# Kernel tuning notes

Hardware: AMD Instinct MI355X
Metric: run time of the kernel (lower is better)

The kernel has to match this reference:

```python
import jax, jax.numpy as jnp
import numpy as np
from jax import lax

H = 256        # hidden_size
T = 576        # history length (PERIOD*24)
F_T = 24       # future steps
M = 32         # m_features
B = 256        # batch
PERIOD = T // 24
E = 2 * H      # encoder output dim (bidirectional)
EPS = 1e-6     # torch PairwiseDistance eps


def setup_inputs() -> dict:
    key = jax.random.key(0)
    ks = jax.random.split(key, 16)
    rn = lambda k, sh, s=1.0: jax.random.normal(k, sh, jnp.float32) * s
    return {
        "input_encoded": rn(ks[0], (B, T, E)),
        "feature_history1": rn(ks[1], (B, T, M)),
        "y_history": rn(ks[2], (B, T, 1)),               # unused by forward (matches torch)
        "feature_future1": rn(ks[3], (B, F_T, M)),
        "hidden": rn(ks[4], (2, B, H), 0.1),
        "cell": rn(ks[5], (2, B, H), 0.1),
        # attn_layer: Linear(2H+M -> T), Tanh, Linear(T -> T)
        "attn_W1": rn(ks[6], (T, E + M), 0.05), "attn_b1": jnp.zeros((T,), jnp.float32),
        "attn_W2": rn(ks[7], (T, T), 0.05),     "attn_b2": jnp.zeros((T,), jnp.float32),
        # bidirectional 1-layer LSTM, stacked over direction d in {fwd, bwd}
        "W_ih": rn(ks[8], (2, 4 * H, E + M), 0.05),
        "W_hh": rn(ks[9], (2, 4 * H, H), 0.05),
        "b_ih": jnp.zeros((2, 4 * H), jnp.float32),
        "b_hh": jnp.zeros((2, 4 * H), jnp.float32),
        # fc_final: Linear(2H -> H), ReLU, Linear(H -> 1)
        "fcf_W1": rn(ks[10], (H, E), 0.05), "fcf_b1": jnp.zeros((H,), jnp.float32),
        "fcf_W2": rn(ks[11], (1, H), 0.05), "fcf_b2": jnp.zeros((1,), jnp.float32),
    }


def reference(input_encoded, feature_history1, y_history, feature_future1,
              hidden, cell, attn_W1, attn_b1, attn_W2, attn_b2,
              W_ih, W_hh, b_ih, b_hh, fcf_W1, fcf_b1, fcf_W2, fcf_b2):
    b = input_encoded.shape[0]
    # --- period-similarity weights alpha (computed once) ---
    fh = feature_history1.reshape(b, PERIOD, 24, M)                 # [B,period,24,M]
    # pairwise L2 distance between future [B,24,1,M] and history hours [B,24,period,M]
    diff = feature_future1[:, :, None, :] - fh.transpose(0, 2, 1, 3)  # [B,24,period,M]
    dist = jnp.sqrt(jnp.sum((diff + EPS) ** 2, axis=-1))            # [B,24,period]
    dp = 1.0 / jnp.sum(dist, axis=2)                                # rsqrt(.)**2 == 1/x; [B,24]
    alpha = jax.nn.softmax(dp, axis=1)                              # [B,24] (period==24)
    enc = input_encoded.reshape(b, PERIOD, 24, E)                   # [B,period,24,E]
    bias = (b_ih + b_hh)[:, None, :]                                # [2,1,4H]

    def step(carry, ff_t):                                          # ff_t: [B,M]
        h, c = carry                                                # each [2,B,H]
        x = jnp.concatenate([h[0], h[1], ff_t], axis=1)             # [B,2H+M]
        a = jnp.tanh(x @ attn_W1.T + attn_b1) @ attn_W2.T + attn_b2
        a = jax.nn.softmax(a, axis=1)                               # [B,T]
        w = a.reshape(b, PERIOD, 24)                                # [B,period,24]
        # context: sum attention-weighted encodings over each day, then alpha over periods
        ctx = jnp.einsum('bpk,bpke,bp->be', w, enc, alpha)          # [B,E]
        inp = jnp.concatenate([ctx, ff_t], axis=1)                  # [B,2H+M]
        gates = (jnp.einsum('bi,dgi->dbg', inp, W_ih)
                 + jnp.einsum('dbh,dgh->dbg', h, W_hh) + bias)      # [2,B,4H]
        i_g, f_g, g_g, o_g = jnp.split(gates, 4, axis=-1)           # torch gate order i,f,g,o
        c_new = jax.nn.sigmoid(f_g) * c + jax.nn.sigmoid(i_g) * jnp.tanh(g_g)
        h_new = jax.nn.sigmoid(o_g) * jnp.tanh(c_new)               # [2,B,H]
        hh = jnp.concatenate([h_new[0], h_new[1]], axis=1)          # [B,2H]
        y = jax.nn.relu(hh @ fcf_W1.T + fcf_b1) @ fcf_W2.T + fcf_b2  # [B,1]
        return (h_new, c_new), y

    _, ys = lax.scan(step, (hidden, cell), jnp.transpose(feature_future1, (1, 0, 2)))
    return jnp.transpose(ys, (1, 0, 2))                             # [B,f_T,1]
```

## Files before the change

### kernel.cpp

```cpp
#include <hip/hip_runtime.h>
#include <math.h>

#define B_ 256
#define T_ 576
#define FT_ 24
#define M_ 32
#define H_ 256
#define E_ 512
#define KX_ 544
#define G_ 1024
#define ND_ 2048
#define EPS_ 1e-6f

typedef __attribute__((ext_vector_type(8))) short bf8;
typedef __attribute__((ext_vector_type(4))) float f4;

__device__ __forceinline__ float bf2f(unsigned short s) {
    union { unsigned u; float f; } c; c.u = ((unsigned)s) << 16; return c.f;
}
__device__ __forceinline__ short f2bf(float f) {
    union { float f; unsigned u; } c; c.f = f;
    unsigned r = c.u + 0x7fffu + ((c.u >> 16) & 1u);
    return (short)(r >> 16);
}
__device__ __forceinline__ float sigm(float x) { return 1.f / (1.f + expf(-x)); }

__global__ __launch_bounds__(64) void k_alpha(const float* __restrict__ ff,
                                              const float* __restrict__ fhist,
                                              float* __restrict__ alpha) {
    int b = blockIdx.x;
    int t = threadIdx.x;
    float dp = 0.f;
    if (t < 24) {
        float fv[M_];
        const float* fp = ff + (b * FT_ + t) * M_;
        #pragma unroll
        for (int m = 0; m < M_; m++) fv[m] = fp[m];
        float dist = 0.f;
        for (int p = 0; p < 24; p++) {
            const float* hp = fhist + (b * T_ + p * 24 + t) * M_;
            float s = 0.f;
            #pragma unroll
            for (int m = 0; m < M_; m++) { float d = fv[m] - hp[m] + EPS_; s += d * d; }
            dist += sqrtf(s);
        }
        dp = 1.f / dist;
    }
    float v = (t < 24) ? dp : -INFINITY;
    float mx = v;
    for (int off = 32; off; off >>= 1) mx = fmaxf(mx, __shfl_xor(mx, off));
    float e = (t < 24) ? expf(dp - mx) : 0.f;
    float sm = e;
    for (int off = 32; off; off >>= 1) sm += __shfl_xor(sm, off);
    if (t < 24) alpha[b * 24 + t] = e / sm;
}

__global__ __launch_bounds__(256) void k_cast4(const float* __restrict__ src,
                                               short* __restrict__ dst, int n4) {
    int i = blockIdx.x * 256 + threadIdx.x;
    if (i < n4) {
        float4 v = ((const float4*)src)[i];
        short4 o;
        o.x = f2bf(v.x); o.y = f2bf(v.y); o.z = f2bf(v.z); o.w = f2bf(v.w);
        ((short4*)dst)[i] = o;
    }
}

__global__ __launch_bounds__(256) void k_init(const float* __restrict__ hidden,
                                              const float* __restrict__ cell,
                                              const float* __restrict__ ff,
                                              short* __restrict__ x, short* __restrict__ hb,
                                              float* __restrict__ c) {
    int i = blockIdx.x * 256 + threadIdx.x;
    int d = i >> 16, b = (i >> 8) & 255, j = i & 255;
    float h = hidden[i];
    short hv = f2bf(h);
    hb[i] = hv;
    x[b * KX_ + d * H_ + j] = hv;
    c[i] = cell[i];
    if (d == 0 && j < M_) x[b * KX_ + E_ + j] = f2bf(ff[(b * FT_ + 0) * M_ + j]);
}

template <int EPI>
__global__ __launch_bounds__(256) void k_gemm(const short* __restrict__ A, int lda, int K,
                                              const short* __restrict__ W,
                                              const float* __restrict__ bias,
                                              void* __restrict__ out, int ldc) {
    __shared__ short As[64][40];
    __shared__ short Bs[64][40];
    int n0 = blockIdx.x * 64, m0 = blockIdx.y * 64;
    int tid = threadIdx.x, lane = tid & 63, w = tid >> 6;
    int wm = (w & 1) * 32, wn = (w >> 1) * 32;
    int r = tid >> 2, cg = (tid & 3) * 8;
    f4 acc[2][2] = {};
    int nch = K / 32;
    int4 pa = *(const int4*)(A + (m0 + r) * lda + cg);
    int4 pb = *(const int4*)(W + (n0 + r) * K + cg);
    for (int kc = 0; kc < nch; kc++) {
        *(int4*)&As[r][cg] = pa;
        *(int4*)&Bs[r][cg] = pb;
        __syncthreads();
        if (kc + 1 < nch) {
            int ko = (kc + 1) * 32 + cg;
            pa = *(const int4*)(A + (m0 + r) * lda + ko);
            pb = *(const int4*)(W + (n0 + r) * K + ko);
        }
        int fr = lane & 15, fk = (lane >> 4) * 8;
        bf8 a0 = *(const bf8*)&As[wm + fr][fk];
        bf8 a1 = *(const bf8*)&As[wm + 16 + fr][fk];
        bf8 b0 = *(const bf8*)&Bs[wn + fr][fk];
        bf8 b1 = *(const bf8*)&Bs[wn + 16 + fr][fk];
        acc[0][0] = __builtin_amdgcn_mfma_f32_16x16x32_bf16(a0, b0, acc[0][0], 0, 0, 0);
        acc[0][1] = __builtin_amdgcn_mfma_f32_16x16x32_bf16(a0, b1, acc[0][1], 0, 0, 0);
        acc[1][0] = __builtin_amdgcn_mfma_f32_16x16x32_bf16(a1, b0, acc[1][0], 0, 0, 0);
        acc[1][1] = __builtin_amdgcn_mfma_f32_16x16x32_bf16(a1, b1, acc[1][1], 0, 0, 0);
        __syncthreads();
    }
    int colb = n0 + wn + (lane & 15);
    int rowb = m0 + wm + (lane >> 4) * 4;
    #pragma unroll
    for (int im = 0; im < 2; im++)
        #pragma unroll
        for (int in = 0; in < 2; in++) {
            int col = colb + in * 16;
            float bv = bias[col];
            #pragma unroll
            for (int q = 0; q < 4; q++) {
                int row = rowb + im * 16 + q;
                float v = acc[im][in][q] + bv;
                if (EPI == 0)      ((short*)out)[row * ldc + col] = f2bf(tanhf(v));
                else if (EPI == 1) ((float*)out)[row * ldc + col] = v;
                else               ((float*)out)[row * ldc + col] = fmaxf(v, 0.f);
            }
        }
}

template <int BF16E>
__global__ __launch_bounds__(256) void k_ctx(const float* __restrict__ logits,
                                             const float* __restrict__ alpha,
                                             const short* __restrict__ encb,
                                             const float* __restrict__ encf,
                                             float* __restrict__ ctxp) {
    int b = blockIdx.x >> 2, s = blockIdx.x & 3;
    int tid = threadIdx.x;
    __shared__ float wt[T_];
    __shared__ float red[4];
    const float* lg = logits + b * T_;
    float l0 = lg[tid], l1 = lg[tid + 256];
    float l2 = (tid < 64) ? lg[tid + 512] : -INFINITY;
    float mx = fmaxf(fmaxf(l0, l1), l2);
    for (int off = 32; off; off >>= 1) mx = fmaxf(mx, __shfl_xor(mx, off));
    if ((tid & 63) == 0) red[tid >> 6] = mx;
    __syncthreads();
    mx = fmaxf(fmaxf(red[0], red[1]), fmaxf(red[2], red[3]));
    float e0 = expf(l0 - mx), e1 = expf(l1 - mx);
    float e2 = (tid < 64) ? expf(l2 - mx) : 0.f;
    float sm = e0 + e1 + e2;
    for (int off = 32; off; off >>= 1) sm += __shfl_xor(sm, off);
    __syncthreads();
    if ((tid & 63) == 0) red[tid >> 6] = sm;
    __syncthreads();
    float inv = 1.f / (red[0] + red[1] + red[2] + red[3]);
    const float* al = alpha + b * 24;
    wt[tid]       = e0 * inv * al[tid / 24];
    wt[tid + 256] = e1 * inv * al[(tid + 256) / 24];
    if (tid < 64) wt[tid + 512] = e2 * inv * al[(tid + 512) / 24];
    __syncthreads();
    float a0 = 0.f, a1 = 0.f;
    int t0 = s * (T_ / 4);
    if (BF16E) {
        const unsigned* ep = (const unsigned*)(encb + (b * T_ + t0) * E_) + tid;
        for (int t = 0; t < T_ / 4; t++) {
            float wv = wt[t0 + t];
            unsigned u = ep[t * (E_ / 2)];
            a0 += wv * bf2f((unsigned short)(u & 0xffffu));
            a1 += wv * bf2f((unsigned short)(u >> 16));
        }
    } else {
        const float2* ep = (const float2*)(encf + ((size_t)b * T_ + t0) * E_) + tid;
        for (int t = 0; t < T_ / 4; t++) {
            float wv = wt[t0 + t];
            float2 u = ep[t * (E_ / 2)];
            a0 += wv * u.x;
            a1 += wv * u.y;
        }
    }
    float* cp = ctxp + (s * B_ + b) * E_;
    cp[2 * tid] = a0;
    cp[2 * tid + 1] = a1;
}

__global__ __launch_bounds__(256) void k_gates(const float* __restrict__ ctxp,
                                               const float* __restrict__ ff, int step,
                                               const short* __restrict__ hb,
                                               const short* __restrict__ Wih,
                                               const short* __restrict__ Whh,
                                               float* __restrict__ gates) {
    __shared__ short As[64][40];
    __shared__ short Bs[64][40];
    int n0 = blockIdx.x * 64, m0 = blockIdx.y * 64;
    int tid = threadIdx.x, lane = tid & 63, w = tid >> 6;
    int wm = (w & 1) * 32, wn = (w >> 1) * 32;
    int r = tid >> 2, cg = (tid & 3) * 8;
    int b = m0 + r;
    f4 acc[2][2] = {};
    int fr = lane & 15, fk = (lane >> 4) * 8;
    for (int kc = 0; kc < KX_ / 32; kc++) {
        int k = kc * 32 + cg;
        short av[8];
        if (k < E_) {
            const float* c0 = ctxp + b * E_ + k;
            #pragma unroll
            for (int j = 0; j < 8; j++) {
                float v = c0[j] + c0[B_ * E_ + j] + c0[2 * B_ * E_ + j] + c0[3 * B_ * E_ + j];
                av[j] = f2bf(v);
            }
        } else {
            const float* fp = ff + (b * FT_ + step) * M_ + (k - E_);
            #pragma unroll
            for (int j = 0; j < 8; j++) av[j] = f2bf(fp[j]);
        }
        *(int4*)&As[r][cg] = *(int4*)av;
        *(int4*)&Bs[r][cg] = *(const int4*)(Wih + (n0 + r) * KX_ + k);
        __syncthreads();
        bf8 a0 = *(const bf8*)&As[wm + fr][fk];
        bf8 a1 = *(const bf8*)&As[wm + 16 + fr][fk];
        bf8 b0 = *(const bf8*)&Bs[wn + fr][fk];
        bf8 b1 = *(const bf8*)&Bs[wn + 16 + fr][fk];
        acc[0][0] = __builtin_amdgcn_mfma_f32_16x16x32_bf16(a0, b0, acc[0][0], 0, 0, 0);
        acc[0][1] = __builtin_amdgcn_mfma_f32_16x16x32_bf16(a0, b1, acc[0][1], 0, 0, 0);
        acc[1][0] = __builtin_amdgcn_mfma_f32_16x16x32_bf16(a1, b0, acc[1][0], 0, 0, 0);
        acc[1][1] = __builtin_amdgcn_mfma_f32_16x16x32_bf16(a1, b1, acc[1][1], 0, 0, 0);
        __syncthreads();
    }
    int d = n0 >> 10;
    const short* A2 = hb + d * B_ * H_;
    for (int kc = 0; kc < H_ / 32; kc++) {
        int k = kc * 32 + cg;
        *(int4*)&As[r][cg] = *(const int4*)(A2 + b * H_ + k);
        *(int4*)&Bs[r][cg] = *(const int4*)(Whh + (n0 + r) * H_ + k);
        __syncthreads();
        bf8 a0 = *(const bf8*)&As[wm + fr][fk];
        bf8 a1 = *(const bf8*)&As[wm + 16 + fr][fk];
        bf8 b0 = *(const bf8*)&Bs[wn + fr][fk];
        bf8 b1 = *(const bf8*)&Bs[wn + 16 + fr][fk];
        acc[0][0] = __builtin_amdgcn_mfma_f32_16x16x32_bf16(a0, b0, acc[0][0], 0, 0, 0);
        acc[0][1] = __builtin_amdgcn_mfma_f32_16x16x32_bf16(a0, b1, acc[0][1], 0, 0, 0);
        acc[1][0] = __builtin_amdgcn_mfma_f32_16x16x32_bf16(a1, b0, acc[1][0], 0, 0, 0);
        acc[1][1] = __builtin_amdgcn_mfma_f32_16x16x32_bf16(a1, b1, acc[1][1], 0, 0, 0);
        __syncthreads();
    }
    int colb = n0 + wn + (lane & 15);
    int rowb = m0 + wm + (lane >> 4) * 4;
    #pragma unroll
    for (int im = 0; im < 2; im++)
        #pragma unroll
        for (int in = 0; in < 2; in++)
            #pragma unroll
            for (int q = 0; q < 4; q++)
                gates[(rowb + im * 16 + q) * ND_ + colb + in * 16] = acc[im][in][q];
}

__global__ __launch_bounds__(256) void k_lstm(const float* __restrict__ gates,
                                              const float* __restrict__ bih,
                                              const float* __restrict__ bhh,
                                              const float* __restrict__ ff, int step,
                                              float* __restrict__ c, short* __restrict__ hb,
                                              short* __restrict__ x) {
    int i = blockIdx.x * 256 + threadIdx.x;
    int d = i >> 16, b = (i >> 8) & 255, j = i & 255;
    int gb = b * ND_ + d * G_;
    int bb = d * G_;
    float ig = gates[gb + j]       + bih[bb + j]       + bhh[bb + j];
    float fg = gates[gb + 256 + j] + bih[bb + 256 + j] + bhh[bb + 256 + j];
    float gg = gates[gb + 512 + j] + bih[bb + 512 + j] + bhh[bb + 512 + j];
    float og = gates[gb + 768 + j] + bih[bb + 768 + j] + bhh[bb + 768 + j];
    float cv = c[i];
    float cn = sigm(fg) * cv + sigm(ig) * tanhf(gg);
    float hn = sigm(og) * tanhf(cn);
    c[i] = cn;
    short hv = f2bf(hn);
    hb[i] = hv;
    x[b * KX_ + d * H_ + j] = hv;
    if (d == 0 && j < M_ && step + 1 < FT_)
        x[b * KX_ + E_ + j] = f2bf(ff[(b * FT_ + step + 1) * M_ + j]);
}

__global__ __launch_bounds__(256) void k_fc2(const float* __restrict__ z,
                                             const float* __restrict__ w2,
                                             const float* __restrict__ b2,
                                             float* __restrict__ out, int step) {
    int b = blockIdx.x * 4 + (threadIdx.x >> 6);
    int lane = threadIdx.x & 63;
    const float* zr = z + b * H_;
    float s = zr[lane] * w2[lane] + zr[lane + 64] * w2[lane + 64] +
              zr[lane + 128] * w2[lane + 128] + zr[lane + 192] * w2[lane + 192];
    for (int off = 32; off; off >>= 1) s += __shfl_xor(s, off);
    if (lane == 0) out[b * FT_ + step] = s + b2[0];
}

extern "C" void kernel_launch(void* const* d_in, const int* in_sizes, int n_in,
                              void* d_out, int out_size, void* d_ws, size_t ws_size,
                              hipStream_t stream) {
    (void)in_sizes; (void)n_in; (void)out_size;
    const float* enc_f  = (const float*)d_in[0];
    const float* fhist  = (const float*)d_in[1];
    const float* ff     = (const float*)d_in[3];
    const float* hidden = (const float*)d_in[4];
    const float* cell   = (const float*)d_in[5];
    const float* aW1    = (const float*)d_in[6];
    const float* ab1    = (const float*)d_in[7];
    const float* aW2    = (const float*)d_in[8];
    const float* ab2    = (const float*)d_in[9];
    const float* Wih    = (const float*)d_in[10];
    const float* Whh    = (const float*)d_in[11];
    const float* bih    = (const float*)d_in[12];
    const float* bhh    = (const float*)d_in[13];
    const float* fW1    = (const float*)d_in[14];
    const float* fb1    = (const float*)d_in[15];
    const float* fW2    = (const float*)d_in[16];
    const float* fb2    = (const float*)d_in[17];
    float* out = (float*)d_out;

    char* p = (char*)d_ws;
    auto take = [&](size_t n) { char* r = p; p += (n + 255) & ~(size_t)255; return r; };
    float* alpha = (float*)take(B_ * 24 * 4);
    short* xb    = (short*)take(B_ * KX_ * 2);
    short* hb    = (short*)take(2 * B_ * H_ * 2);
    float* cbuf  = (float*)take(2 * B_ * H_ * 4);
    short* s1    = (short*)take(B_ * T_ * 2);
    float* logit = (float*)take(B_ * T_ * 4);
    float* ctxp  = (float*)take(4 * B_ * E_ * 4);
    float* gates = (float*)take(B_ * ND_ * 4);
    float* z     = (float*)take(B_ * H_ * 4);
    short* W1b   = (short*)take(T_ * KX_ * 2);
    short* W2b   = (short*)take(T_ * T_ * 2);
    short* Wihb  = (short*)take(ND_ * KX_ * 2);
    short* Whhb  = (short*)take(ND_ * H_ * 2);
    short* fW1b  = (short*)take(H_ * E_ * 2);
    short* encb  = (short*)take((size_t)B_ * T_ * E_ * 2);
    size_t full_need = (size_t)(p - (char*)d_ws);
    bool use_encb = ws_size >= full_need;

    k_alpha<<<B_, 64, 0, stream>>>(ff, fhist, alpha);
    k_cast4<<<(T_ * KX_ / 4 + 255) / 256, 256, 0, stream>>>(aW1, W1b, T_ * KX_ / 4);
    k_cast4<<<(T_ * T_ / 4 + 255) / 256, 256, 0, stream>>>(aW2, W2b, T_ * T_ / 4);
    k_cast4<<<(ND_ * KX_ / 4 + 255) / 256, 256, 0, stream>>>(Wih, Wihb, ND_ * KX_ / 4);
    k_cast4<<<(ND_ * H_ / 4 + 255) / 256, 256, 0, stream>>>(Whh, Whhb, ND_ * H_ / 4);
    k_cast4<<<(H_ * E_ / 4 + 255) / 256, 256, 0, stream>>>(fW1, fW1b, H_ * E_ / 4);
    if (use_encb)
        k_cast4<<<(B_ * T_ * E_ / 4 + 255) / 256, 256, 0, stream>>>(enc_f, encb, B_ * T_ * E_ / 4);
    k_init<<<(2 * B_ * H_) / 256, 256, 0, stream>>>(hidden, cell, ff, xb, hb, cbuf);

    for (int step = 0; step < FT_; step++) {
        k_gemm<0><<<dim3(T_ / 64, B_ / 64), 256, 0, stream>>>(xb, KX_, KX_, W1b, ab1, s1, T_);
        k_gemm<1><<<dim3(T_ / 64, B_ / 64), 256, 0, stream>>>(s1, T_, T_, W2b, ab2, logit, T_);
        if (use_encb)
            k_ctx<1><<<B_ * 4, 256, 0, stream>>>(logit, alpha, encb, enc_f, ctxp);
        else
            k_ctx<0><<<B_ * 4, 256, 0, stream>>>(logit, alpha, encb, enc_f, ctxp);
        k_gates<<<dim3(ND_ / 64, B_ / 64), 256, 0, stream>>>(ctxp, ff, step, hb, Wihb, Whhb, gates);
        k_lstm<<<(2 * B_ * H_) / 256, 256, 0, stream>>>(gates, bih, bhh, ff, step, cbuf, hb, xb);
        k_gemm<3><<<dim3(H_ / 64, B_ / 64), 256, 0, stream>>>(xb, KX_, E_, fW1b, fb1, z, H_);
        k_fc2<<<B_ / 4, 256, 0, stream>>>(z, fW2, fb2, out, step);
    }
}
```

Before: 2.283 ms.

## Fuse setup casts, gate GEMM with LSTM cell, and FC head into fewer kernels

All one-time conversion and init kernels are merged into a single grid-stride setup kernel. The LSTM weights are reordered so the i,f,g,o gates for one hidden unit sit in adjacent columns, which lets the gate GEMM kernel apply the LSTM cell update straight from shared memory. That removes the gates buffer round trip and one launch per step, and h is ping-ponged between two buffers to avoid read/write races across blocks. The FC head GEMM now does ReLU and the dot with fW2 in its epilogue and accumulates into the output with atomics, and the GEMM K-tile grows from 32 to 64. The changes trade extra atomics and a 16-block FC launch against fewer launches and less global traffic.

Result: slower. 2.397 ms (+5.0%).

```diff
diff --git a/kernel.cpp b/kernel.cpp
--- a/kernel.cpp
+++ b/kernel.cpp
@@ -8,9 +8,9 @@
 #define H_ 256
 #define E_ 512
 #define KX_ 544
-#define G_ 1024
 #define ND_ 2048
 #define EPS_ 1e-6f
+#define LDAS 72
 
 typedef __attribute__((ext_vector_type(8))) short bf8;
 typedef __attribute__((ext_vector_type(4))) float f4;
@@ -25,60 +25,132 @@
 }
 __device__ __forceinline__ float sigm(float x) { return 1.f / (1.f + expf(-x)); }
 
-__global__ __launch_bounds__(64) void k_alpha(const float* __restrict__ ff,
-                                              const float* __restrict__ fhist,
-                                              float* __restrict__ alpha) {
-    int b = blockIdx.x;
-    int t = threadIdx.x;
-    float dp = 0.f;
-    if (t < 24) {
-        float fv[M_];
-        const float* fp = ff + (b * FT_ + t) * M_;
-        #pragma unroll
-        for (int m = 0; m < M_; m++) fv[m] = fp[m];
-        float dist = 0.f;
-        for (int p = 0; p < 24; p++) {
-            const float* hp = fhist + (b * T_ + p * 24 + t) * M_;
-            float s = 0.f;
-            #pragma unroll
-            for (int m = 0; m < M_; m++) { float d = fv[m] - hp[m] + EPS_; s += d * d; }
-            dist += sqrtf(s);
-        }
-        dp = 1.f / dist;
-    }
-    float v = (t < 24) ? dp : -INFINITY;
-    float mx = v;
-    for (int off = 32; off; off >>= 1) mx = fmaxf(mx, __shfl_xor(mx, off));
-    float e = (t < 24) ? expf(dp - mx) : 0.f;
-    float sm = e;
-    for (int off = 32; off; off >>= 1) sm += __shfl_xor(sm, off);
-    if (t < 24) alpha[b * 24 + t] = e / sm;
-}
-
-__global__ __launch_bounds__(256) void k_cast4(const float* __restrict__ src,
-                                               short* __restrict__ dst, int n4) {
-    int i = blockIdx.x * 256 + threadIdx.x;
-    if (i < n4) {
-        float4 v = ((const float4*)src)[i];
-        short4 o;
-        o.x = f2bf(v.x); o.y = f2bf(v.y); o.z = f2bf(v.z); o.w = f2bf(v.w);
-        ((short4*)dst)[i] = o;
-    }
-}
-
-__global__ __launch_bounds__(256) void k_init(const float* __restrict__ hidden,
-                                              const float* __restrict__ cell,
-                                              const float* __restrict__ ff,
-                                              short* __restrict__ x, short* __restrict__ hb,
-                                              float* __restrict__ c) {
-    int i = blockIdx.x * 256 + threadIdx.x;
-    int d = i >> 16, b = (i >> 8) & 255, j = i & 255;
-    float h = hidden[i];
-    short hv = f2bf(h);
-    hb[i] = hv;
-    x[b * KX_ + d * H_ + j] = hv;
-    c[i] = cell[i];
-    if (d == 0 && j < M_) x[b * KX_ + E_ + j] = f2bf(ff[(b * FT_ + 0) * M_ + j]);
+__device__ __forceinline__ void mfma4(const short (*As)[LDAS], const short (*Bs)[LDAS],
+                                      int wm, int wn, int fr, int fk, f4 acc[2][2]) {
+    bf8 a0 = *(const bf8*)&As[wm + fr][fk];
+    bf8 a1 = *(const bf8*)&As[wm + 16 + fr][fk];
+    bf8 b0 = *(const bf8*)&Bs[wn + fr][fk];
+    bf8 b1 = *(const bf8*)&Bs[wn + 16 + fr][fk];
+    acc[0][0] = __builtin_amdgcn_mfma_f32_16x16x32_bf16(a0, b0, acc[0][0], 0, 0, 0);
+    acc[0][1] = __builtin_amdgcn_mfma_f32_16x16x32_bf16(a0, b1, acc[0][1], 0, 0, 0);
+    acc[1][0] = __builtin_amdgcn_mfma_f32_16x16x32_bf16(a1, b0, acc[1][0], 0, 0, 0);
+    acc[1][1] = __builtin_amdgcn_mfma_f32_16x16x32_bf16(a1, b1, acc[1][1], 0, 0, 0);
+}
+
+__device__ __forceinline__ void gemm64(const short* __restrict__ A, int lda,
+                                       const short* __restrict__ Wt, int ldw, int K,
+                                       short (*As)[LDAS], short (*Bs)[LDAS], int tid,
+                                       f4 acc[2][2]) {
+    int lane = tid & 63, w = tid >> 6;
+    int wm = (w & 1) * 32, wn = (w >> 1) * 32;
+    int fr = lane & 15, fk = (lane >> 4) * 8;
+    int r = tid >> 2, c0 = (tid & 3) * 16, c8 = (tid & 3) * 8;
+    int4 pa0, pa1, pb0, pb1;
+    auto ld = [&](int k0) {
+        if (K - k0 >= 64) {
+            pa0 = *(const int4*)(A + r * lda + k0 + c0);
+            pa1 = *(const int4*)(A + r * lda + k0 + c0 + 8);
+            pb0 = *(const int4*)(Wt + r * ldw + k0 + c0);
+            pb1 = *(const int4*)(Wt + r * ldw + k0 + c0 + 8);
+        } else {
+            pa0 = *(const int4*)(A + r * lda + k0 + c8);
+            pb0 = *(const int4*)(Wt + r * ldw + k0 + c8);
+        }
+    };
+    ld(0);
+    for (int k0 = 0; k0 < K; k0 += 64) {
+        int rem = K - k0;
+        if (rem >= 64) {
+            *(int4*)&As[r][c0] = pa0; *(int4*)&As[r][c0 + 8] = pa1;
+            *(int4*)&Bs[r][c0] = pb0; *(int4*)&Bs[r][c0 + 8] = pb1;
+        } else {
+            *(int4*)&As[r][c8] = pa0;
+            *(int4*)&Bs[r][c8] = pb0;
+        }
+        __syncthreads();
+        if (k0 + 64 < K) ld(k0 + 64);
+        mfma4(As, Bs, wm, wn, fr, fk, acc);
+        if (rem >= 64) mfma4(As, Bs, wm, wn, fr, fk + 32, acc);
+        __syncthreads();
+    }
+}
+
+struct SetupPrm {
+    const float *enc, *fhist, *ff, *hidden, *cell;
+    const float *aW1, *aW2, *Wih, *Whh, *bih, *bhh, *fW1;
+    short *W1b, *W2b, *Wihb, *Whhb, *fW1b, *encb, *xb, *hA;
+    float *bcomb, *alpha, *cbuf;
+};
+
+__global__ __launch_bounds__(256) void k_setup(SetupPrm p) {
+    const int NT = 2048 * 256;
+    int gt = blockIdx.x * 256 + threadIdx.x;
+    auto cast = [&](const float* s, short* d, int n4) {
+        for (int i = gt; i < n4; i += NT) {
+            float4 v = ((const float4*)s)[i];
+            short4 o; o.x = f2bf(v.x); o.y = f2bf(v.y); o.z = f2bf(v.z); o.w = f2bf(v.w);
+            ((short4*)d)[i] = o;
+        }
+    };
+    cast(p.aW1, p.W1b, T_ * KX_ / 4);
+    cast(p.aW2, p.W2b, T_ * T_ / 4);
+    cast(p.fW1, p.fW1b, H_ * E_ / 4);
+    cast(p.enc, p.encb, B_ * T_ * E_ / 4);
+    for (int i = gt; i < ND_ * KX_ / 4; i += NT) {
+        int row = i / (KX_ / 4), c4 = i % (KX_ / 4);
+        int d = row >> 10, rest = row & 1023, j = rest >> 2, g = rest & 3;
+        int orig = d * 1024 + g * 256 + j;
+        float4 v = ((const float4*)(p.Wih + orig * KX_))[c4];
+        short4 o; o.x = f2bf(v.x); o.y = f2bf(v.y); o.z = f2bf(v.z); o.w = f2bf(v.w);
+        ((short4*)(p.Wihb + row * KX_))[c4] = o;
+    }
+    for (int i = gt; i < ND_ * H_ / 4; i += NT) {
+        int row = i / (H_ / 4), c4 = i % (H_ / 4);
+        int d = row >> 10, rest = row & 1023, j = rest >> 2, g = rest & 3;
+        int orig = d * 1024 + g * 256 + j;
+        float4 v = ((const float4*)(p.Whh + orig * H_))[c4];
+        short4 o; o.x = f2bf(v.x); o.y = f2bf(v.y); o.z = f2bf(v.z); o.w = f2bf(v.w);
+        ((short4*)(p.Whhb + row * H_))[c4] = o;
+    }
+    for (int i = gt; i < ND_; i += NT) {
+        int d = i >> 10, rest = i & 1023, j = rest >> 2, g = rest & 3;
+        int orig = d * 1024 + g * 256 + j;
+        p.bcomb[i] = p.bih[orig] + p.bhh[orig];
+    }
+    for (int i = gt; i < 2 * B_ * H_; i += NT) {
+        int d = i >> 16, b = (i >> 8) & 255, j = i & 255;
+        short hv = f2bf(p.hidden[i]);
+        p.xb[b * KX_ + d * H_ + j] = hv;
+        p.hA[i] = hv;
+        p.cbuf[i] = p.cell[i];
+        if (d == 0 && j < M_) p.xb[b * KX_ + E_ + j] = f2bf(p.ff[b * FT_ * M_ + j]);
+    }
+    if (blockIdx.x < 256 && threadIdx.x < 64) {
+        int b = blockIdx.x, t = threadIdx.x;
+        float dp = 0.f;
+        if (t < 24) {
+            float fv[M_];
+            const float* fp = p.ff + (b * FT_ + t) * M_;
+            #pragma unroll
+            for (int m = 0; m < M_; m++) fv[m] = fp[m];
+            float dist = 0.f;
+            for (int pp = 0; pp < 24; pp++) {
+                const float* hp = p.fhist + (b * T_ + pp * 24 + t) * M_;
+                float s = 0.f;
+                #pragma unroll
+                for (int m = 0; m < M_; m++) { float d = fv[m] - hp[m] + EPS_; s += d * d; }
+                dist += sqrtf(s);
+            }
+            dp = 1.f / dist;
+        }
+        float v = (t < 24) ? dp : -INFINITY;
+        float mx = v;
+        for (int off = 32; off; off >>= 1) mx = fmaxf(mx, __shfl_xor(mx, off));
+        float e = (t < 24) ? expf(dp - mx) : 0.f;
+        float sme = e;
+        for (int off = 32; off; off >>= 1) sme += __shfl_xor(sme, off);
+        if (t < 24) p.alpha[b * 24 + t] = e / sme;
+    }
 }
 
 template <int EPI>
@@ -86,36 +158,13 @@
                                               const short* __restrict__ W,
                                               const float* __restrict__ bias,
                                               void* __restrict__ out, int ldc) {
-    __shared__ short As[64][40];
-    __shared__ short Bs[64][40];
-    int n0 = blockIdx.x * 64, m0 = blockIdx.y * 64;
-    int tid = threadIdx.x, lane = tid & 63, w = tid >> 6;
+    __shared__ short As[64][LDAS];
+    __shared__ short Bs[64][LDAS];
+    int n0 = blockIdx.x * 64, m0 = blockIdx.y * 64, tid = threadIdx.x;
+    f4 acc[2][2] = {};
+    gemm64(A + m0 * lda, lda, W + n0 * K, K, K, As, Bs, tid, acc);
+    int lane = tid & 63, w = tid >> 6;
     int wm = (w & 1) * 32, wn = (w >> 1) * 32;
-    int r = tid >> 2, cg = (tid & 3) * 8;
-    f4 acc[2][2] = {};
-    int nch = K / 32;
-    int4 pa = *(const int4*)(A + (m0 + r) * lda + cg);
-    int4 pb = *(const int4*)(W + (n0 + r) * K + cg);
-    for (int kc = 0; kc < nch; kc++) {
-        *(int4*)&As[r][cg] = pa;
-        *(int4*)&Bs[r][cg] = pb;
-        __syncthreads();
-        if (kc + 1 < nch) {
-            int ko = (kc + 1) * 32 + cg;
-            pa = *(const int4*)(A + (m0 + r) * lda + ko);
-            pb = *(const int4*)(W + (n0 + r) * K + ko);
-        }
-        int fr = lane & 15, fk = (lane >> 4) * 8;
-        bf8 a0 = *(const bf8*)&As[wm + fr][fk];
-        bf8 a1 = *(const bf8*)&As[wm + 16 + fr][fk];
-        bf8 b0 = *(const bf8*)&Bs[wn + fr][fk];
-        bf8 b1 = *(const bf8*)&Bs[wn + 16 + fr][fk];
-        acc[0][0] = __builtin_amdgcn_mfma_f32_16x16x32_bf16(a0, b0, acc[0][0], 0, 0, 0);
-        acc[0][1] = __builtin_amdgcn_mfma_f32_16x16x32_bf16(a0, b1, acc[0][1], 0, 0, 0);
-        acc[1][0] = __builtin_amdgcn_mfma_f32_16x16x32_bf16(a1, b0, acc[1][0], 0, 0, 0);
-        acc[1][1] = __builtin_amdgcn_mfma_f32_16x16x32_bf16(a1, b1, acc[1][1], 0, 0, 0);
-        __syncthreads();
-    }
     int colb = n0 + wn + (lane & 15);
     int rowb = m0 + wm + (lane >> 4) * 4;
     #pragma unroll
@@ -128,18 +177,15 @@
             for (int q = 0; q < 4; q++) {
                 int row = rowb + im * 16 + q;
                 float v = acc[im][in][q] + bv;
-                if (EPI == 0)      ((short*)out)[row * ldc + col] = f2bf(tanhf(v));
-                else if (EPI == 1) ((float*)out)[row * ldc + col] = v;
-                else               ((float*)out)[row * ldc + col] = fmaxf(v, 0.f);
+                if (EPI == 0) ((short*)out)[row * ldc + col] = f2bf(tanhf(v));
+                else          ((float*)out)[row * ldc + col] = v;
             }
         }
 }
 
-template <int BF16E>
 __global__ __launch_bounds__(256) void k_ctx(const float* __restrict__ logits,
                                              const float* __restrict__ alpha,
                                              const short* __restrict__ encb,
-                                             const float* __restrict__ encf,
                                              float* __restrict__ ctxp) {
     int b = blockIdx.x >> 2, s = blockIdx.x & 3;
     int tid = threadIdx.x;
@@ -155,10 +201,10 @@
     mx = fmaxf(fmaxf(red[0], red[1]), fmaxf(red[2], red[3]));
     float e0 = expf(l0 - mx), e1 = expf(l1 - mx);
     float e2 = (tid < 64) ? expf(l2 - mx) : 0.f;
-    float sm = e0 + e1 + e2;
-    for (int off = 32; off; off >>= 1) sm += __shfl_xor(sm, off);
-    __syncthreads();
-    if ((tid & 63) == 0) red[tid >> 6] = sm;
+    float sme = e0 + e1 + e2;
+    for (int off = 32; off; off >>= 1) sme += __shfl_xor(sme, off);
+    __syncthreads();
+    if ((tid & 63) == 0) red[tid >> 6] = sme;
     __syncthreads();
     float inv = 1.f / (red[0] + red[1] + red[2] + red[3]);
     const float* al = alpha + b * 24;
@@ -168,141 +214,144 @@
     __syncthreads();
     float a0 = 0.f, a1 = 0.f;
     int t0 = s * (T_ / 4);
-    if (BF16E) {
-        const unsigned* ep = (const unsigned*)(encb + (b * T_ + t0) * E_) + tid;
-        for (int t = 0; t < T_ / 4; t++) {
-            float wv = wt[t0 + t];
-            unsigned u = ep[t * (E_ / 2)];
-            a0 += wv * bf2f((unsigned short)(u & 0xffffu));
-            a1 += wv * bf2f((unsigned short)(u >> 16));
-        }
-    } else {
-        const float2* ep = (const float2*)(encf + ((size_t)b * T_ + t0) * E_) + tid;
-        for (int t = 0; t < T_ / 4; t++) {
-            float wv = wt[t0 + t];
-            float2 u = ep[t * (E_ / 2)];
-            a0 += wv * u.x;
-            a1 += wv * u.y;
-        }
+    const unsigned* ep = (const unsigned*)(encb + ((size_t)b * T_ + t0) * E_) + tid;
+    #pragma unroll 8
+    for (int t = 0; t < T_ / 4; t++) {
+        float wv = wt[t0 + t];
+        unsigned u = ep[(size_t)t * (E_ / 2)];
+        a0 += wv * bf2f((unsigned short)(u & 0xffffu));
+        a1 += wv * bf2f((unsigned short)(u >> 16));
     }
     float* cp = ctxp + (s * B_ + b) * E_;
     cp[2 * tid] = a0;
     cp[2 * tid + 1] = a1;
 }
 
-__global__ __launch_bounds__(256) void k_gates(const float* __restrict__ ctxp,
-                                               const float* __restrict__ ff, int step,
-                                               const short* __restrict__ hb,
-                                               const short* __restrict__ Wih,
-                                               const short* __restrict__ Whh,
-                                               float* __restrict__ gates) {
-    __shared__ short As[64][40];
-    __shared__ short Bs[64][40];
-    int n0 = blockIdx.x * 64, m0 = blockIdx.y * 64;
-    int tid = threadIdx.x, lane = tid & 63, w = tid >> 6;
+__global__ __launch_bounds__(256) void k_gl(const float* __restrict__ ctxp,
+                                            const float* __restrict__ ff, int t,
+                                            short* __restrict__ xb,
+                                            const short* __restrict__ Wihb,
+                                            const short* __restrict__ Whhb,
+                                            const float* __restrict__ bcomb,
+                                            float* __restrict__ cbuf,
+                                            const short* __restrict__ hprev,
+                                            short* __restrict__ hnext,
+                                            const float* __restrict__ fb2,
+                                            float* __restrict__ out) {
+    __shared__ union {
+        struct { short As[64][LDAS]; short Bs[64][LDAS]; } g;
+        float gt[64][68];
+    } sm;
+    int n0 = blockIdx.x * 64, m0 = blockIdx.y * 64, tid = threadIdx.x;
+    int lane = tid & 63, w = tid >> 6;
     int wm = (w & 1) * 32, wn = (w >> 1) * 32;
-    int r = tid >> 2, cg = (tid & 3) * 8;
-    int b = m0 + r;
+    int fr = lane & 15, fk = (lane >> 4) * 8;
+    int r = tid >> 2, c0 = (tid & 3) * 16, c8 = (tid & 3) * 8;
     f4 acc[2][2] = {};
-    int fr = lane & 15, fk = (lane >> 4) * 8;
-    for (int kc = 0; kc < KX_ / 32; kc++) {
-        int k = kc * 32 + cg;
-        short av[8];
-        if (k < E_) {
-            const float* c0 = ctxp + b * E_ + k;
-            #pragma unroll
-            for (int j = 0; j < 8; j++) {
-                float v = c0[j] + c0[B_ * E_ + j] + c0[2 * B_ * E_ + j] + c0[3 * B_ * E_ + j];
-                av[j] = f2bf(v);
-            }
+    for (int k0 = 0; k0 < KX_; k0 += 64) {
+        int rem = KX_ - k0;
+        if (rem >= 64) {
+            const float* cp = ctxp + (m0 + r) * E_ + k0 + c0;
+            short av[16];
+            #pragma unroll
+            for (int i = 0; i < 16; i++)
+                av[i] = f2bf(cp[i] + cp[B_ * E_ + i] + cp[2 * B_ * E_ + i] + cp[3 * B_ * E_ + i]);
+            *(int4*)&sm.g.As[r][c0]     = *(int4*)&av[0];
+            *(int4*)&sm.g.As[r][c0 + 8] = *(int4*)&av[8];
+            *(int4*)&sm.g.Bs[r][c0]     = *(const int4*)(Wihb + (n0 + r) * KX_ + k0 + c0);
+            *(int4*)&sm.g.Bs[r][c0 + 8] = *(const int4*)(Wihb + (n0 + r) * KX_ + k0 + c0 + 8);
         } else {
-            const float* fp = ff + (b * FT_ + step) * M_ + (k - E_);
-            #pragma unroll
-            for (int j = 0; j < 8; j++) av[j] = f2bf(fp[j]);
-        }
-        *(int4*)&As[r][cg] = *(int4*)av;
-        *(int4*)&Bs[r][cg] = *(const int4*)(Wih + (n0 + r) * KX_ + k);
+            const float* fp = ff + ((m0 + r) * FT_ + t) * M_ + (k0 + c8 - E_);
+            short av[8];
+            #pragma unroll
+            for (int i = 0; i < 8; i++) av[i] = f2bf(fp[i]);
+            *(int4*)&sm.g.As[r][c8] = *(int4*)&av[0];
+            *(int4*)&sm.g.Bs[r][c8] = *(const int4*)(Wihb + (n0 + r) * KX_ + k0 + c8);
+        }
         __syncthreads();
-        bf8 a0 = *(const bf8*)&As[wm + fr][fk];
-        bf8 a1 = *(const bf8*)&As[wm + 16 + fr][fk];
-        bf8 b0 = *(const bf8*)&Bs[wn + fr][fk];
-        bf8 b1 = *(const bf8*)&Bs[wn + 16 + fr][fk];
-        acc[0][0] = __builtin_amdgcn_mfma_f32_16x16x32_bf16(a0, b0, acc[0][0], 0, 0, 0);
-        acc[0][1] = __builtin_amdgcn_mfma_f32_16x16x32_bf16(a0, b1, acc[0][1], 0, 0, 0);
-        acc[1][0] = __builtin_amdgcn_mfma_f32_16x16x32_bf16(a1, b0, acc[1][0], 0, 0, 0);
-        acc[1][1] = __builtin_amdgcn_mfma_f32_16x16x32_bf16(a1, b1, acc[1][1], 0, 0, 0);
+        mfma4(sm.g.As, sm.g.Bs, wm, wn, fr, fk, acc);
+        if (rem >= 64) mfma4(sm.g.As, sm.g.Bs, wm, wn, fr, fk + 32, acc);
         __syncthreads();
     }
     int d = n0 >> 10;
-    const short* A2 = hb + d * B_ * H_;
-    for (int kc = 0; kc < H_ / 32; kc++) {
-        int k = kc * 32 + cg;
-        *(int4*)&As[r][cg] = *(const int4*)(A2 + b * H_ + k);
-        *(int4*)&Bs[r][cg] = *(const int4*)(Whh + (n0 + r) * H_ + k);
-        __syncthreads();
-        bf8 a0 = *(const bf8*)&As[wm + fr][fk];
-        bf8 a1 = *(const bf8*)&As[wm + 16 + fr][fk];
-        bf8 b0 = *(const bf8*)&Bs[wn + fr][fk];
-        bf8 b1 = *(const bf8*)&Bs[wn + 16 + fr][fk];
-        acc[0][0] = __builtin_amdgcn_mfma_f32_16x16x32_bf16(a0, b0, acc[0][0], 0, 0, 0);
-        acc[0][1] = __builtin_amdgcn_mfma_f32_16x16x32_bf16(a0, b1, acc[0][1], 0, 0, 0);
-        acc[1][0] = __builtin_amdgcn_mfma_f32_16x16x32_bf16(a1, b0, acc[1][0], 0, 0, 0);
-        acc[1][1] = __builtin_amdgcn_mfma_f32_16x16x32_bf16(a1, b1, acc[1][1], 0, 0, 0);
-        __syncthreads();
-    }
-    int colb = n0 + wn + (lane & 15);
-    int rowb = m0 + wm + (lane >> 4) * 4;
+    gemm64(hprev + d * B_ * H_ + m0 * H_, H_, Whhb + n0 * H_, H_, H_,
+           sm.g.As, sm.g.Bs, tid, acc);
+    int clb = wn + (lane & 15);
+    int rlb = wm + (lane >> 4) * 4;
     #pragma unroll
     for (int im = 0; im < 2; im++)
         #pragma unroll
-        for (int in = 0; in < 2; in++)
+        for (int in = 0; in < 2; in++) {
+            int cl = clb + in * 16;
+            float bv = bcomb[n0 + cl];
             #pragma unroll
             for (int q = 0; q < 4; q++)
-                gates[(rowb + im * 16 + q) * ND_ + colb + in * 16] = acc[im][in][q];
-}
-
-__global__ __launch_bounds__(256) void k_lstm(const float* __restrict__ gates,
-                                              const float* __restrict__ bih,
-                                              const float* __restrict__ bhh,
-                                              const float* __restrict__ ff, int step,
-                                              float* __restrict__ c, short* __restrict__ hb,
-                                              short* __restrict__ x) {
-    int i = blockIdx.x * 256 + threadIdx.x;
-    int d = i >> 16, b = (i >> 8) & 255, j = i & 255;
-    int gb = b * ND_ + d * G_;
-    int bb = d * G_;
-    float ig = gates[gb + j]       + bih[bb + j]       + bhh[bb + j];
-    float fg = gates[gb + 256 + j] + bih[bb + 256 + j] + bhh[bb + 256 + j];
-    float gg = gates[gb + 512 + j] + bih[bb + 512 + j] + bhh[bb + 512 + j];
-    float og = gates[gb + 768 + j] + bih[bb + 768 + j] + bhh[bb + 768 + j];
-    float cv = c[i];
-    float cn = sigm(fg) * cv + sigm(ig) * tanhf(gg);
-    float hn = sigm(og) * tanhf(cn);
-    c[i] = cn;
-    short hv = f2bf(hn);
-    hb[i] = hv;
-    x[b * KX_ + d * H_ + j] = hv;
-    if (d == 0 && j < M_ && step + 1 < FT_)
-        x[b * KX_ + E_ + j] = f2bf(ff[(b * FT_ + step + 1) * M_ + j]);
-}
-
-__global__ __launch_bounds__(256) void k_fc2(const float* __restrict__ z,
-                                             const float* __restrict__ w2,
-                                             const float* __restrict__ b2,
-                                             float* __restrict__ out, int step) {
-    int b = blockIdx.x * 4 + (threadIdx.x >> 6);
-    int lane = threadIdx.x & 63;
-    const float* zr = z + b * H_;
-    float s = zr[lane] * w2[lane] + zr[lane + 64] * w2[lane + 64] +
-              zr[lane + 128] * w2[lane + 128] + zr[lane + 192] * w2[lane + 192];
-    for (int off = 32; off; off >>= 1) s += __shfl_xor(s, off);
-    if (lane == 0) out[b * FT_ + step] = s + b2[0];
+                sm.gt[rlb + im * 16 + q][cl] = acc[im][in][q] + bv;
+        }
+    __syncthreads();
+    int j0 = (n0 >> 2) & 255;
+    #pragma unroll
+    for (int it = 0; it < 4; it++) {
+        int item = tid + it * 256;
+        int rl = item >> 4, ql = item & 15;
+        float ig = sm.gt[rl][ql * 4 + 0];
+        float fg = sm.gt[rl][ql * 4 + 1];
+        float gg = sm.gt[rl][ql * 4 + 2];
+        float og = sm.gt[rl][ql * 4 + 3];
+        int b = m0 + rl, j = j0 + ql;
+        int ci = d * 65536 + b * 256 + j;
+        float cn = sigm(fg) * cbuf[ci] + sigm(ig) * tanhf(gg);
+        float hn = sigm(og) * tanhf(cn);
+        cbuf[ci] = cn;
+        short hv = f2bf(hn);
+        xb[b * KX_ + d * H_ + j] = hv;
+        hnext[ci] = hv;
+        if (d == 0 && j < M_ && t + 1 < FT_)
+            xb[b * KX_ + E_ + j] = f2bf(ff[(b * FT_ + t + 1) * M_ + j]);
+        if (n0 == 0 && ql == 0) out[b * FT_ + t] = fb2[0];
+    }
+}
+
+__global__ __launch_bounds__(256) void k_fc(const short* __restrict__ xb,
+                                            const short* __restrict__ fW1b,
+                                            const float* __restrict__ fb1,
+                                            const float* __restrict__ fW2,
+                                            float* __restrict__ out, int step) {
+    __shared__ short As[64][LDAS];
+    __shared__ short Bs[64][LDAS];
+    __shared__ float ypart[64];
+    int fb = blockIdx.x, tid = threadIdx.x;
+    int m0 = (fb >> 2) * 64, n0 = (fb & 3) * 64;
+    f4 acc[2][2] = {};
+    gemm64(xb + m0 * KX_, KX_, fW1b + n0 * E_, E_, E_, As, Bs, tid, acc);
+    if (tid < 64) ypart[tid] = 0.f;
+    __syncthreads();
+    int lane = tid & 63, w = tid >> 6;
+    int wm = (w & 1) * 32, wn = (w >> 1) * 32;
+    int colb = n0 + wn + (lane & 15);
+    int rloc = wm + (lane >> 4) * 4;
+    #pragma unroll
+    for (int im = 0; im < 2; im++)
+        #pragma unroll
+        for (int q = 0; q < 4; q++) {
+            float s = 0.f;
+            #pragma unroll
+            for (int in = 0; in < 2; in++) {
+                int col = colb + in * 16;
+                s += fmaxf(acc[im][in][q] + fb1[col], 0.f) * fW2[col];
+            }
+            #pragma unroll
+            for (int off = 1; off < 16; off <<= 1) s += __shfl_xor(s, off);
+            if ((lane & 15) == 0) atomicAdd(&ypart[rloc + im * 16 + q], s);
+        }
+    __syncthreads();
+    if (tid < 64) atomicAdd(&out[(m0 + tid) * FT_ + step], ypart[tid]);
 }
 
 extern "C" void kernel_launch(void* const* d_in, const int* in_sizes, int n_in,
                               void* d_out, int out_size, void* d_ws, size_t ws_size,
                               hipStream_t stream) {
-    (void)in_sizes; (void)n_in; (void)out_size;
+    (void)in_sizes; (void)n_in; (void)out_size; (void)ws_size;
     const float* enc_f  = (const float*)d_in[0];
     const float* fhist  = (const float*)d_in[1];
     const float* ff     = (const float*)d_in[3];
@@ -322,46 +371,42 @@
     const float* fb2    = (const float*)d_in[17];
     float* out = (float*)d_out;
 
-    char* p = (char*)d_ws;
-    auto take = [&](size_t n) { char* r = p; p += (n + 255) & ~(size_t)255; return r; };
+    char* pws = (char*)d_ws;
+    auto take = [&](size_t n) { char* r = pws; pws += (n + 255) & ~(size_t)255; return r; };
     float* alpha = (float*)take(B_ * 24 * 4);
     short* xb    = (short*)take(B_ * KX_ * 2);
-    short* hb    = (short*)take(2 * B_ * H_ * 2);
+    short* hA    = (short*)take(2 * B_ * H_ * 2);
+    short* hB    = (short*)take(2 * B_ * H_ * 2);
     float* cbuf  = (float*)take(2 * B_ * H_ * 4);
     short* s1    = (short*)take(B_ * T_ * 2);
     float* logit = (float*)take(B_ * T_ * 4);
     float* ctxp  = (float*)take(4 * B_ * E_ * 4);
-    float* gates = (float*)take(B_ * ND_ * 4);
-    float* z     = (float*)take(B_ * H_ * 4);
+    float* bcomb = (float*)take(ND_ * 4);
     short* W1b   = (short*)take(T_ * KX_ * 2);
     short* W2b   = (short*)take(T_ * T_ * 2);
     short* Wihb  = (short*)take(ND_ * KX_ * 2);
     short* Whhb  = (short*)take(ND_ * H_ * 2);
     short* fW1b  = (short*)take(H_ * E_ * 2);
     short* encb  = (short*)take((size_t)B_ * T_ * E_ * 2);
-    size_t full_need = (size_t)(p - (char*)d_ws);
-    bool use_encb = ws_size >= full_need;
-
-    k_alpha<<<B_, 64, 0, stream>>>(ff, fhist, alpha);
-    k_cast4<<<(T_ * KX_ / 4 + 255) / 256, 256, 0, stream>>>(aW1, W1b, T_ * KX_ / 4);
-    k_cast4<<<(T_ * T_ / 4 + 255) / 256, 256, 0, stream>>>(aW2, W2b, T_ * T_ / 4);
-    k_cast4<<<(ND_ * KX_ / 4 + 255) / 256, 256, 0, stream>>>(Wih, Wihb, ND_ * KX_ / 4);
-    k_cast4<<<(ND_ * H_ / 4 + 255) / 256, 256, 0, stream>>>(Whh, Whhb, ND_ * H_ / 4);
-    k_cast4<<<(H_ * E_ / 4 + 255) / 256, 256, 0, stream>>>(fW1, fW1b, H_ * E_ / 4);
-    if (use_encb)
-        k_cast4<<<(B_ * T_ * E_ / 4 + 255) / 256, 256, 0, stream>>>(enc_f, encb, B_ * T_ * E_ / 4);
-    k_init<<<(2 * B_ * H_) / 256, 256, 0, stream>>>(hidden, cell, ff, xb, hb, cbuf);
-
-    for (int step = 0; step < FT_; step++) {
+
+    SetupPrm sp;
+    sp.enc = enc_f; sp.fhist = fhist; sp.ff = ff; sp.hidden = hidden; sp.cell = cell;
+    sp.aW1 = aW1; sp.aW2 = aW2; sp.Wih = Wih; sp.Whh = Whh; sp.bih = bih; sp.bhh = bhh;
+    sp.fW1 = fW1;
+    sp.W1b = W1b; sp.W2b = W2b; sp.Wihb = Wihb; sp.Whhb = Whhb; sp.fW1b = fW1b;
+    sp.encb = encb; sp.xb = xb; sp.hA = hA;
+    sp.bcomb = bcomb; sp.alpha = alpha; sp.cbuf = cbuf;
+
+    k_setup<<<2048, 256, 0, stream>>>(sp);
+
+    for (int t = 0; t < FT_; t++) {
         k_gemm<0><<<dim3(T_ / 64, B_ / 64), 256, 0, stream>>>(xb, KX_, KX_, W1b, ab1, s1, T_);
         k_gemm<1><<<dim3(T_ / 64, B_ / 64), 256, 0, stream>>>(s1, T_, T_, W2b, ab2, logit, T_);
-        if (use_encb)
-            k_ctx<1><<<B_ * 4, 256, 0, stream>>>(logit, alpha, encb, enc_f, ctxp);
-        else
-            k_ctx<0><<<B_ * 4, 256, 0, stream>>>(logit, alpha, encb, enc_f, ctxp);
-        k_gates<<<dim3(ND_ / 64, B_ / 64), 256, 0, stream>>>(ctxp, ff, step, hb, Wihb, Whhb, gates);
-        k_lstm<<<(2 * B_ * H_) / 256, 256, 0, stream>>>(gates, bih, bhh, ff, step, cbuf, hb, xb);
-        k_gemm<3><<<dim3(H_ / 64, B_ / 64), 256, 0, stream>>>(xb, KX_, E_, fW1b, fb1, z, H_);
-        k_fc2<<<B_ / 4, 256, 0, stream>>>(z, fW2, fb2, out, step);
-    }
-}
+        k_ctx<<<B_ * 4, 256, 0, stream>>>(logit, alpha, encb, ctxp);
+        const short* hprev = (t & 1) ? hB : hA;
+        short* hnext       = (t & 1) ? hA : hB;
+        k_gl<<<dim3(ND_ / 64, B_ / 64), 256, 0, stream>>>(ctxp, ff, t, xb, Wihb, Whhb,
+                                                          bcomb, cbuf, hprev, hnext, fb2, out);
+        k_fc<<<16, 256, 0, stream>>>(xb, fW1b, fb1, fW2, out, t);
+    }
+}
```
